# Optimization experiments

Hardware: AMD Instinct MI355X
Metric: run time of the kernel (lower is better)

Reference implementation:

```python
import jax, jax.numpy as jnp
import numpy as np
import math

N = 12288
IN_MAIN, IN_MOD = 64, 128
NC_INNER, NC_QK, OUT_MAIN = 16, 8, 64

def setup_inputs() -> dict:
    key = jax.random.key(0)
    ks = jax.random.split(key, 8)
    s = lambda fan_in: 1.0 / np.sqrt(fan_in)
    return {
        "x_main": jax.random.normal(ks[0], (N, IN_MAIN), dtype=jnp.float32),
        "x_mod": jax.random.normal(ks[1], (N, IN_MOD), dtype=jnp.float32),
        "xyz": jax.random.uniform(ks[2], (N, 3), dtype=jnp.float32),
        # MLP E: [in_main+in_mod -> nc_inner -> nc_inner], bias=False (weights stored [in, out])
        "W_e1": jax.random.uniform(ks[3], (IN_MAIN + IN_MOD, NC_INNER), jnp.float32, -s(IN_MAIN + IN_MOD), s(IN_MAIN + IN_MOD)),
        "W_e2": jax.random.uniform(ks[4], (NC_INNER, NC_INNER), jnp.float32, -s(NC_INNER), s(NC_INNER)),
        "W_q": jax.random.uniform(ks[5], (NC_INNER, NC_QK), jnp.float32, -s(NC_INNER), s(NC_INNER)),
        "W_k": jax.random.uniform(ks[6], (NC_INNER, NC_QK), jnp.float32, -s(NC_INNER), s(NC_INNER)),
        "W_v": jax.random.uniform(ks[7], (NC_INNER, OUT_MAIN), jnp.float32, -s(NC_INNER), s(NC_INNER)),
    }

def reference(x_main, x_mod, xyz, W_e1, W_e2, W_q, W_k, W_v):
    # concat 3D + 2D features: [N, in_main+in_mod]
    x = jnp.concatenate((x_main, x_mod), axis=-1)
    # MLP E (bias-free Linear + ReLU per layer): [N, nc_inner]
    h = jax.nn.relu(jax.nn.relu(x @ W_e1) @ W_e2)
    Q = h @ W_q  # [N, nc_qk]
    K = h @ W_k  # [N, nc_qk]
    V = h @ W_v  # [N, out_main]
    scale = 1.0 / math.sqrt(NC_QK)
    scores = (Q @ K.T) * scale          # [N, N] full global attention
    attn = jax.nn.softmax(scores, axis=1)
    return attn @ V                     # [N, out_main]
```

## Files before the change

### kernel.cpp

```cpp
#include <hip/hip_runtime.h>
#include <stdint.h>


#define NN 12288

typedef float    f32x16 __attribute__((ext_vector_type(16)));
typedef short    s16x8  __attribute__((ext_vector_type(8)));
typedef unsigned short u16;

#define MFMA_32x32x16_BF16 __builtin_amdgcn_mfma_f32_32x32x16_bf16

#define OFF_QB   0u
#define OFF_KB   196608u
#define OFF_VT   393216u
#define OFF_PO   2162688u

typedef __attribute__((address_space(3))) void lds_void_t;
typedef const __attribute__((address_space(1))) void gbl_void_t;
__device__ __forceinline__ void gld16(const void* g, void* l) {
    __builtin_amdgcn_global_load_lds((gbl_void_t*)g, (lds_void_t*)l, 16, 0, 0);
}

__device__ __forceinline__ float bf2f(u16 s) {
    union { unsigned int u; float f; } c; c.u = ((unsigned int)s) << 16; return c.f;
}
__device__ __forceinline__ u16 f2bf(float f) {
    union { float f; unsigned int u; } c; c.f = f;
    return (u16)((c.u + 0x8000u) >> 16);
}
__device__ __forceinline__ unsigned int pk2(float a, float b) {
    union { float f; unsigned int u; } ca, cb; ca.f = a; cb.f = b;
    return ((ca.u + 0x8000u) >> 16) | ((cb.u + 0x8000u) & 0xffff0000u);
}
__device__ __forceinline__ unsigned int pkbf(float a, float b) {
#if __has_builtin(__builtin_amdgcn_cvt_pk_bf16_f32)
    auto r = __builtin_amdgcn_cvt_pk_bf16_f32(a, b);
    union { decltype(r) v; unsigned int u; } c; c.v = r; return c.u;
#else
    return pk2(a, b);
#endif
}
__device__ __forceinline__ f32x16 zf16() {
    f32x16 z;
#pragma unroll
    for (int i = 0; i < 16; ++i) z[i] = 0.f;
    return z;
}
__device__ __forceinline__ s16x8 zs8() {
    s16x8 z;
#pragma unroll
    for (int i = 0; i < 8; ++i) z[i] = 0;
    return z;
}

union U8 { s16x8 v; unsigned int u[4]; };

__global__ __launch_bounds__(256) void k1_qkv(
    const void* __restrict__ xmain, const void* __restrict__ xmod,
    const void* __restrict__ we1, const void* __restrict__ we2,
    const void* __restrict__ wqp, const void* __restrict__ wkp,
    const void* __restrict__ wvp,
    u16* __restrict__ qb, u16* __restrict__ kb, u16* __restrict__ vt)
{
    __shared__ float wf[4608];
    __shared__ int   sflag;
    __shared__ float lh1[64][4][17];
    __shared__ float lh2[64][17];

    const int t = threadIdx.x;
    const int r = t >> 2;
    const int p = t & 3;
    const int row = blockIdx.x * 64 + r;

    if (t == 0) sflag = 0;
    __syncthreads();
    {
        float v = bf2f(((const u16*)xmod)[2 * t]);
        if (fabsf(v) > 16.f) atomicAdd(&sflag, 1);
    }
    __syncthreads();
    const int isf32 = (sflag > 8);

    const float SCL = 0.51006979f;
    if (isf32) {
        const float* a1 = (const float*)we1; const float* a2 = (const float*)we2;
        const float* aq = (const float*)wqp; const float* ak = (const float*)wkp;
        const float* av = (const float*)wvp;
        for (int i = t; i < 4608; i += 256) {
            if      (i < 3072) wf[i] = a1[i];
            else if (i < 3328) wf[i] = a2[i - 3072];
            else if (i < 3456) wf[i] = aq[i - 3328] * SCL;
            else if (i < 3584) wf[i] = ak[i - 3456];
            else               wf[i] = av[i - 3584];
        }
    } else {
        const u16* a1 = (const u16*)we1; const u16* a2 = (const u16*)we2;
        const u16* aq = (const u16*)wqp; const u16* ak = (const u16*)wkp;
        const u16* av = (const u16*)wvp;
        for (int i = t; i < 4608; i += 256) {
            if      (i < 3072) wf[i] = bf2f(a1[i]);
            else if (i < 3328) wf[i] = bf2f(a2[i - 3072]);
            else if (i < 3456) wf[i] = bf2f(aq[i - 3328]) * SCL;
            else if (i < 3584) wf[i] = bf2f(ak[i - 3456]);
            else               wf[i] = bf2f(av[i - 3584]);
        }
    }
    __syncthreads();

    const float* __restrict__ W1 = wf;
    const float* __restrict__ W2 = wf + 3072;
    const float* __restrict__ Wq = wf + 3328;
    const float* __restrict__ Wk = wf + 3456;
    const float* __restrict__ Wv = wf + 3584;

    float h1p[16];
#pragma unroll
    for (int o = 0; o < 16; ++o) h1p[o] = 0.f;

    if (isf32) {
#pragma unroll
        for (int cc = 0; cc < 12; ++cc) {
            const int c = p + cc * 4;
            float4 xv = (c < 16)
                ? ((const float4*)xmain)[(size_t)row * 16 + c]
                : ((const float4*)xmod)[(size_t)row * 32 + (c - 16)];
            float xs[4] = {xv.x, xv.y, xv.z, xv.w};
#pragma unroll
            for (int j = 0; j < 4; ++j) {
                const float* wr = W1 + (c * 4 + j) * 16;
#pragma unroll
                for (int o = 0; o < 16; ++o) h1p[o] += xs[j] * wr[o];
            }
        }
    } else {
#pragma unroll
        for (int cc = 0; cc < 12; ++cc) {
            const int c = p + cc * 4;
            uint2 xv = (c < 16)
                ? ((const uint2*)xmain)[(size_t)row * 16 + c]
                : ((const uint2*)xmod)[(size_t)row * 32 + (c - 16)];
            float xs[4] = { bf2f((u16)(xv.x & 0xffff)), bf2f((u16)(xv.x >> 16)),
                            bf2f((u16)(xv.y & 0xffff)), bf2f((u16)(xv.y >> 16)) };
#pragma unroll
            for (int j = 0; j < 4; ++j) {
                const float* wr = W1 + (c * 4 + j) * 16;
#pragma unroll
                for (int o = 0; o < 16; ++o) h1p[o] += xs[j] * wr[o];
            }
        }
    }
#pragma unroll
    for (int o = 0; o < 16; ++o) lh1[r][p][o] = h1p[o];
    __syncthreads();

    float h1[16];
#pragma unroll
    for (int o = 0; o < 16; ++o)
        h1[o] = fmaxf(lh1[r][0][o] + lh1[r][1][o] + lh1[r][2][o] + lh1[r][3][o], 0.f);

#pragma unroll
    for (int oo = 0; oo < 4; ++oo) {
        const int o = p * 4 + oo;
        float s = 0.f;
#pragma unroll
        for (int j = 0; j < 16; ++j) s += h1[j] * W2[j * 16 + o];
        lh2[r][o] = fmaxf(s, 0.f);
    }
    __syncthreads();

    float h2[16];
#pragma unroll
    for (int j = 0; j < 16; ++j) h2[j] = lh2[r][j];

    {
        float q0 = 0.f, q1 = 0.f, k0 = 0.f, k1 = 0.f;
        const int o = 2 * p;
#pragma unroll
        for (int j = 0; j < 16; ++j) {
            q0 += h2[j] * Wq[j * 8 + o];
            q1 += h2[j] * Wq[j * 8 + o + 1];
            k0 += h2[j] * Wk[j * 8 + o];
            k1 += h2[j] * Wk[j * 8 + o + 1];
        }
        ((unsigned int*)qb)[(size_t)row * 4 + p] = pk2(q0, q1);
        ((unsigned int*)kb)[(size_t)row * 4 + p] = pk2(k0, k1);
    }

    const int tI = row >> 5, kk = row & 31;
#pragma unroll
    for (int c16 = 0; c16 < 16; ++c16) {
        const int c = p * 16 + c16;
        float v = 0.f;
#pragma unroll
        for (int j = 0; j < 16; ++j) v += h2[j] * Wv[j * 64 + c];
        vt[(size_t)tI * 2304 + c * 36 + kk] = f2bf(v);
    }
}

__global__ __launch_bounds__(256, 6) void k2_attn(
    const u16* __restrict__ qb, const u16* __restrict__ kb,
    const u16* __restrict__ vt,
    u16* __restrict__ po, float* __restrict__ pl,
    int nsplit, int tiles)
{
    __shared__ union SM {
        uint4 stage[2][288];
        float sf[2304];
    } sm;

    const int tid  = threadIdx.x;
    const int lane = tid & 63;
    const int half = lane >> 5;
    const int l31  = lane & 31;
    const int w    = tid >> 6;
    const int qB   = (blockIdx.x % 96) * 128;
    const int sp   = blockIdx.x / 96;
    const int myq  = qB + 32 * w;
    const int key_start = sp * (NN / nsplit);
    const int t0 = key_start >> 5;

    const f32x16 Z = zf16();
    s16x8 qf = zs8();
    if (!half) qf = *(const s16x8*)(qb + (size_t)(myq + l31) * 8);

    f32x16 acc0 = Z, acc1 = Z;
    float ls = 0.f;

    {
        const char* g = (const char*)vt + (size_t)t0 * 4608 + 1152 * w + lane * 16;
        char* l = (char*)&sm.stage[0][0] + 1152 * w;
        gld16(g, l);
        if (lane < 8) gld16(g + 1024, l + 1024);
    }
    s16x8 ka_c = *(const s16x8*)(kb + (size_t)(key_start + l31) * 8);

    for (int kt = 0; kt < tiles; ++kt) {
        __builtin_amdgcn_s_waitcnt(0x0F70);
        __syncthreads();
        const int cb = kt & 1;
        const bool has_next = (kt + 1 < tiles);

        s16x8 ka_n;
        if (has_next) {
            ka_n = *(const s16x8*)(kb + (size_t)(key_start + (kt + 1) * 32 + l31) * 8);
            const char* g = (const char*)vt + (size_t)(t0 + kt + 1) * 4608
                          + 1152 * w + lane * 16;
            char* l = (char*)&sm.stage[cb ^ 1][0] + 1152 * w;
            gld16(g, l);
            if (lane < 8) gld16(g + 1024, l + 1024);
        }

        f32x16 S = MFMA_32x32x16_BF16(ka_c, qf, Z, 0, 0, 0);

        float pr[16];
        float ls0 = 0.f, ls1 = 0.f;
#pragma unroll
        for (int r = 0; r < 8; ++r) {
            pr[r]     = __builtin_amdgcn_exp2f(S[r]);
            pr[r + 8] = __builtin_amdgcn_exp2f(S[r + 8]);
            ls0 += pr[r];
            ls1 += pr[r + 8];
        }
        ls += ls0 + ls1;

        U8 pb0, pb1;
#pragma unroll
        for (int i = 0; i < 4; ++i) {
            pb0.u[i] = pkbf(pr[2 * i],     pr[2 * i + 1]);
            pb1.u[i] = pkbf(pr[8 + 2 * i], pr[8 + 2 * i + 1]);
        }

        const u16* base = (const u16*)&sm.stage[cb][0];
        const u16* r0 = base + l31 * 36 + 4 * half;
        const u16* r1 = base + (32 + l31) * 36 + 4 * half;
        U8 va;
        uint2 x0, x1;
        x0 = *(const uint2*)(r0);       x1 = *(const uint2*)(r0 + 8);
        va.u[0] = x0.x; va.u[1] = x0.y; va.u[2] = x1.x; va.u[3] = x1.y;
        acc0 = MFMA_32x32x16_BF16(va.v, pb0.v, acc0, 0, 0, 0);
        x0 = *(const uint2*)(r1);       x1 = *(const uint2*)(r1 + 8);
        va.u[0] = x0.x; va.u[1] = x0.y; va.u[2] = x1.x; va.u[3] = x1.y;
        acc1 = MFMA_32x32x16_BF16(va.v, pb0.v, acc1, 0, 0, 0);
        x0 = *(const uint2*)(r0 + 16);  x1 = *(const uint2*)(r0 + 24);
        va.u[0] = x0.x; va.u[1] = x0.y; va.u[2] = x1.x; va.u[3] = x1.y;
        acc0 = MFMA_32x32x16_BF16(va.v, pb1.v, acc0, 0, 0, 0);
        x0 = *(const uint2*)(r1 + 16);  x1 = *(const uint2*)(r1 + 24);
        va.u[0] = x0.x; va.u[1] = x0.y; va.u[2] = x1.x; va.u[3] = x1.y;
        acc1 = MFMA_32x32x16_BF16(va.v, pb1.v, acc1, 0, 0, 0);

        if (has_next) ka_c = ka_n;
    }

    ls += __shfl_xor(ls, 32, 64);

    u16* poS = po + (size_t)sp * (NN * 64);
    for (int j = 0; j < 4; ++j) {
        __syncthreads();
        if (w == j) {
#pragma unroll
            for (int r = 0; r < 16; ++r) {
                const int c = (r & 3) + 8 * (r >> 2) + 4 * half;
                sm.sf[c * 33 + l31]        = acc0[r];
                sm.sf[(32 + c) * 33 + l31] = acc1[r];
            }
            if (lane < 32) sm.sf[2112 + l31] = ls;
        }
        __syncthreads();
        const int rq = tid >> 3;
        const int c0 = (tid & 7) * 8;
        unsigned int u0 = pkbf(sm.sf[(c0 + 0) * 33 + rq], sm.sf[(c0 + 1) * 33 + rq]);
        unsigned int u1 = pkbf(sm.sf[(c0 + 2) * 33 + rq], sm.sf[(c0 + 3) * 33 + rq]);
        unsigned int u2 = pkbf(sm.sf[(c0 + 4) * 33 + rq], sm.sf[(c0 + 5) * 33 + rq]);
        unsigned int u3 = pkbf(sm.sf[(c0 + 6) * 33 + rq], sm.sf[(c0 + 7) * 33 + rq]);
        *(uint4*)(poS + (size_t)(qB + 32 * j + rq) * 64 + c0) =
            make_uint4(u0, u1, u2, u3);
        if (tid < 32)
            pl[(size_t)sp * NN + qB + 32 * j + tid] = sm.sf[2112 + tid];
    }
}

__global__ __launch_bounds__(256) void k3_norm(
    const u16* __restrict__ po, const float* __restrict__ pl,
    float4* __restrict__ out, int nsplit)
{
    const int i = blockIdx.x * 256 + threadIdx.x;
    const int row = i >> 4;
    const int c0 = (i & 15) * 4;
    float l = 0.f;
    float o0 = 0.f, o1 = 0.f, o2 = 0.f, o3 = 0.f;
    for (int s = 0; s < nsplit; ++s) {
        l += pl[(size_t)s * NN + row];
        uint2 p = *(const uint2*)(po + (size_t)s * (NN * 64) +
                                  (size_t)row * 64 + c0);
        o0 += bf2f((u16)(p.x & 0xffff)); o1 += bf2f((u16)(p.x >> 16));
        o2 += bf2f((u16)(p.y & 0xffff)); o3 += bf2f((u16)(p.y >> 16));
    }
    const float rl = 1.0f / l;
    out[i] = make_float4(o0 * rl, o1 * rl, o2 * rl, o3 * rl);
}

extern "C" void kernel_launch(void* const* d_in, const int* in_sizes, int n_in,
                              void* d_out, int out_size, void* d_ws, size_t ws_size,
                              hipStream_t stream)
{
    const void* xmain = d_in[0];
    const void* xmod  = d_in[1];
    const void* we1   = d_in[3];
    const void* we2   = d_in[4];
    const void* wq    = d_in[5];
    const void* wk    = d_in[6];
    const void* wv    = d_in[7];

    char* ws = (char*)d_ws;
    u16*   qb   = (u16*)  (ws + OFF_QB);
    u16*   kb   = (u16*)  (ws + OFF_KB);
    u16*   vt   = (u16*)  (ws + OFF_VT);

    int S = 1;
    for (int cand = 16; cand >= 1; cand >>= 1) {
        size_t need = (size_t)OFF_PO + (size_t)cand * (NN * 64 * 2) +
                      (size_t)cand * (NN * 4);
        if (ws_size >= need) { S = cand; break; }
    }
    u16*   po = (u16*)(ws + OFF_PO);
    float* pl = (float*)(ws + OFF_PO + (size_t)S * (NN * 64 * 2));
    const int tiles = NN / (32 * S);

    k1_qkv<<<192, 256, 0, stream>>>(xmain, xmod, we1, we2, wq, wk, wv,
                                    qb, kb, vt);
    k2_attn<<<96 * S, 256, 0, stream>>>(qb, kb, vt, po, pl, S, tiles);
    k3_norm<<<768, 256, 0, stream>>>(po, pl, (float4*)d_out, S);
}
```

Measured before the change: 131.2 us.

## Process two query tiles per wave to reuse staged V and K fragments

Each attention wave now handles 64 queries (two 32-row Q fragments), so every K fragment load and every staged V tile in LDS feeds twice as many MFMAs. The grid halves to 48*S blocks and the occupancy hint drops from 6 to 2 to leave room for four accumulators. The QKV projection kernel is also re-split to 32 rows per block with 8 threads per row, giving more blocks. The trade is fewer resident waves and a longer per-wave dependency chain, in exchange for less LDS and global traffic per unit of work.

```diff
diff --git a/kernel.cpp b/kernel.cpp
--- a/kernel.cpp
+++ b/kernel.cpp
@@ -64,13 +64,13 @@
 {
     __shared__ float wf[4608];
     __shared__ int   sflag;
-    __shared__ float lh1[64][4][17];
-    __shared__ float lh2[64][17];
+    __shared__ float lh1[32][8][17];
+    __shared__ float lh2[32][17];
 
     const int t = threadIdx.x;
-    const int r = t >> 2;
-    const int p = t & 3;
-    const int row = blockIdx.x * 64 + r;
+    const int r = t >> 3;
+    const int p = t & 7;
+    const int row = blockIdx.x * 32 + r;
 
     if (t == 0) sflag = 0;
     __syncthreads();
@@ -119,8 +119,8 @@
 
     if (isf32) {
 #pragma unroll
-        for (int cc = 0; cc < 12; ++cc) {
-            const int c = p + cc * 4;
+        for (int cc = 0; cc < 6; ++cc) {
+            const int c = p + cc * 8;
             float4 xv = (c < 16)
                 ? ((const float4*)xmain)[(size_t)row * 16 + c]
                 : ((const float4*)xmod)[(size_t)row * 32 + (c - 16)];
@@ -134,8 +134,8 @@
         }
     } else {
 #pragma unroll
-        for (int cc = 0; cc < 12; ++cc) {
-            const int c = p + cc * 4;
+        for (int cc = 0; cc < 6; ++cc) {
+            const int c = p + cc * 8;
             uint2 xv = (c < 16)
                 ? ((const uint2*)xmain)[(size_t)row * 16 + c]
                 : ((const uint2*)xmod)[(size_t)row * 32 + (c - 16)];
@@ -155,12 +155,16 @@
 
     float h1[16];
 #pragma unroll
-    for (int o = 0; o < 16; ++o)
-        h1[o] = fmaxf(lh1[r][0][o] + lh1[r][1][o] + lh1[r][2][o] + lh1[r][3][o], 0.f);
-
-#pragma unroll
-    for (int oo = 0; oo < 4; ++oo) {
-        const int o = p * 4 + oo;
+    for (int o = 0; o < 16; ++o) {
+        float s = lh1[r][0][o];
+#pragma unroll
+        for (int q = 1; q < 8; ++q) s += lh1[r][q][o];
+        h1[o] = fmaxf(s, 0.f);
+    }
+
+#pragma unroll
+    for (int oo = 0; oo < 2; ++oo) {
+        const int o = p * 2 + oo;
         float s = 0.f;
 #pragma unroll
         for (int j = 0; j < 16; ++j) s += h1[j] * W2[j * 16 + o];
@@ -173,23 +177,23 @@
     for (int j = 0; j < 16; ++j) h2[j] = lh2[r][j];
 
     {
-        float q0 = 0.f, q1 = 0.f, k0 = 0.f, k1 = 0.f;
-        const int o = 2 * p;
+        const int isK = p >> 2;
+        const int o = 2 * (p & 3);
+        const float* Wx = isK ? Wk : Wq;
+        float a0 = 0.f, a1 = 0.f;
 #pragma unroll
         for (int j = 0; j < 16; ++j) {
-            q0 += h2[j] * Wq[j * 8 + o];
-            q1 += h2[j] * Wq[j * 8 + o + 1];
-            k0 += h2[j] * Wk[j * 8 + o];
-            k1 += h2[j] * Wk[j * 8 + o + 1];
-        }
-        ((unsigned int*)qb)[(size_t)row * 4 + p] = pk2(q0, q1);
-        ((unsigned int*)kb)[(size_t)row * 4 + p] = pk2(k0, k1);
+            a0 += h2[j] * Wx[j * 8 + o];
+            a1 += h2[j] * Wx[j * 8 + o + 1];
+        }
+        unsigned int* dst = isK ? (unsigned int*)kb : (unsigned int*)qb;
+        dst[(size_t)row * 4 + (p & 3)] = pk2(a0, a1);
     }
 
     const int tI = row >> 5, kk = row & 31;
 #pragma unroll
-    for (int c16 = 0; c16 < 16; ++c16) {
-        const int c = p * 16 + c16;
+    for (int c8 = 0; c8 < 8; ++c8) {
+        const int c = p * 8 + c8;
         float v = 0.f;
 #pragma unroll
         for (int j = 0; j < 16; ++j) v += h2[j] * Wv[j * 64 + c];
@@ -197,7 +201,7 @@
     }
 }
 
-__global__ __launch_bounds__(256, 6) void k2_attn(
+__global__ __launch_bounds__(256, 2) void k2_attn(
     const u16* __restrict__ qb, const u16* __restrict__ kb,
     const u16* __restrict__ vt,
     u16* __restrict__ po, float* __restrict__ pl,
@@ -213,18 +217,21 @@
     const int half = lane >> 5;
     const int l31  = lane & 31;
     const int w    = tid >> 6;
-    const int qB   = (blockIdx.x % 96) * 128;
-    const int sp   = blockIdx.x / 96;
-    const int myq  = qB + 32 * w;
+    const int qB   = (blockIdx.x % 48) * 256;
+    const int sp   = blockIdx.x / 48;
+    const int myq  = qB + 64 * w;
     const int key_start = sp * (NN / nsplit);
     const int t0 = key_start >> 5;
 
     const f32x16 Z = zf16();
-    s16x8 qf = zs8();
-    if (!half) qf = *(const s16x8*)(qb + (size_t)(myq + l31) * 8);
-
-    f32x16 acc0 = Z, acc1 = Z;
-    float ls = 0.f;
+    s16x8 qf0 = zs8(), qf1 = zs8();
+    if (!half) {
+        qf0 = *(const s16x8*)(qb + (size_t)(myq + l31) * 8);
+        qf1 = *(const s16x8*)(qb + (size_t)(myq + 32 + l31) * 8);
+    }
+
+    f32x16 acc00 = Z, acc01 = Z, acc10 = Z, acc11 = Z;
+    float ls0 = 0.f, ls1 = 0.f;
 
     {
         const char* g = (const char*)vt + (size_t)t0 * 4608 + 1152 * w + lane * 16;
@@ -250,60 +257,85 @@
             if (lane < 8) gld16(g + 1024, l + 1024);
         }
 
-        f32x16 S = MFMA_32x32x16_BF16(ka_c, qf, Z, 0, 0, 0);
-
-        float pr[16];
-        float ls0 = 0.f, ls1 = 0.f;
-#pragma unroll
-        for (int r = 0; r < 8; ++r) {
-            pr[r]     = __builtin_amdgcn_exp2f(S[r]);
-            pr[r + 8] = __builtin_amdgcn_exp2f(S[r + 8]);
-            ls0 += pr[r];
-            ls1 += pr[r + 8];
-        }
-        ls += ls0 + ls1;
-
-        U8 pb0, pb1;
-#pragma unroll
-        for (int i = 0; i < 4; ++i) {
-            pb0.u[i] = pkbf(pr[2 * i],     pr[2 * i + 1]);
-            pb1.u[i] = pkbf(pr[8 + 2 * i], pr[8 + 2 * i + 1]);
-        }
-
         const u16* base = (const u16*)&sm.stage[cb][0];
         const u16* r0 = base + l31 * 36 + 4 * half;
         const u16* r1 = base + (32 + l31) * 36 + 4 * half;
-        U8 va;
-        uint2 x0, x1;
-        x0 = *(const uint2*)(r0);       x1 = *(const uint2*)(r0 + 8);
-        va.u[0] = x0.x; va.u[1] = x0.y; va.u[2] = x1.x; va.u[3] = x1.y;
-        acc0 = MFMA_32x32x16_BF16(va.v, pb0.v, acc0, 0, 0, 0);
-        x0 = *(const uint2*)(r1);       x1 = *(const uint2*)(r1 + 8);
-        va.u[0] = x0.x; va.u[1] = x0.y; va.u[2] = x1.x; va.u[3] = x1.y;
-        acc1 = MFMA_32x32x16_BF16(va.v, pb0.v, acc1, 0, 0, 0);
-        x0 = *(const uint2*)(r0 + 16);  x1 = *(const uint2*)(r0 + 24);
-        va.u[0] = x0.x; va.u[1] = x0.y; va.u[2] = x1.x; va.u[3] = x1.y;
-        acc0 = MFMA_32x32x16_BF16(va.v, pb1.v, acc0, 0, 0, 0);
-        x0 = *(const uint2*)(r1 + 16);  x1 = *(const uint2*)(r1 + 24);
-        va.u[0] = x0.x; va.u[1] = x0.y; va.u[2] = x1.x; va.u[3] = x1.y;
-        acc1 = MFMA_32x32x16_BF16(va.v, pb1.v, acc1, 0, 0, 0);
+        U8 vaA0, vaA1, vaB0, vaB1;
+        {
+            uint2 x0, x1;
+            x0 = *(const uint2*)(r0);       x1 = *(const uint2*)(r0 + 8);
+            vaA0.u[0] = x0.x; vaA0.u[1] = x0.y; vaA0.u[2] = x1.x; vaA0.u[3] = x1.y;
+            x0 = *(const uint2*)(r1);       x1 = *(const uint2*)(r1 + 8);
+            vaA1.u[0] = x0.x; vaA1.u[1] = x0.y; vaA1.u[2] = x1.x; vaA1.u[3] = x1.y;
+            x0 = *(const uint2*)(r0 + 16);  x1 = *(const uint2*)(r0 + 24);
+            vaB0.u[0] = x0.x; vaB0.u[1] = x0.y; vaB0.u[2] = x1.x; vaB0.u[3] = x1.y;
+            x0 = *(const uint2*)(r1 + 16);  x1 = *(const uint2*)(r1 + 24);
+            vaB1.u[0] = x0.x; vaB1.u[1] = x0.y; vaB1.u[2] = x1.x; vaB1.u[3] = x1.y;
+        }
+
+        {
+            f32x16 S = MFMA_32x32x16_BF16(ka_c, qf0, Z, 0, 0, 0);
+            float pr[16];
+            float a = 0.f, b = 0.f;
+#pragma unroll
+            for (int r = 0; r < 8; ++r) {
+                pr[r]     = __builtin_amdgcn_exp2f(S[r]);
+                pr[r + 8] = __builtin_amdgcn_exp2f(S[r + 8]);
+                a += pr[r]; b += pr[r + 8];
+            }
+            ls0 += a + b;
+            U8 pbA, pbB;
+#pragma unroll
+            for (int i = 0; i < 4; ++i) {
+                pbA.u[i] = pkbf(pr[2 * i],     pr[2 * i + 1]);
+                pbB.u[i] = pkbf(pr[8 + 2 * i], pr[8 + 2 * i + 1]);
+            }
+            acc00 = MFMA_32x32x16_BF16(vaA0.v, pbA.v, acc00, 0, 0, 0);
+            acc01 = MFMA_32x32x16_BF16(vaA1.v, pbA.v, acc01, 0, 0, 0);
+            acc00 = MFMA_32x32x16_BF16(vaB0.v, pbB.v, acc00, 0, 0, 0);
+            acc01 = MFMA_32x32x16_BF16(vaB1.v, pbB.v, acc01, 0, 0, 0);
+        }
+        {
+            f32x16 S = MFMA_32x32x16_BF16(ka_c, qf1, Z, 0, 0, 0);
+            float pr[16];
+            float a = 0.f, b = 0.f;
+#pragma unroll
+            for (int r = 0; r < 8; ++r) {
+                pr[r]     = __builtin_amdgcn_exp2f(S[r]);
+                pr[r + 8] = __builtin_amdgcn_exp2f(S[r + 8]);
+                a += pr[r]; b += pr[r + 8];
+            }
+            ls1 += a + b;
+            U8 pbA, pbB;
+#pragma unroll
+            for (int i = 0; i < 4; ++i) {
+                pbA.u[i] = pkbf(pr[2 * i],     pr[2 * i + 1]);
+                pbB.u[i] = pkbf(pr[8 + 2 * i], pr[8 + 2 * i + 1]);
+            }
+            acc10 = MFMA_32x32x16_BF16(vaA0.v, pbA.v, acc10, 0, 0, 0);
+            acc11 = MFMA_32x32x16_BF16(vaA1.v, pbA.v, acc11, 0, 0, 0);
+            acc10 = MFMA_32x32x16_BF16(vaB0.v, pbB.v, acc10, 0, 0, 0);
+            acc11 = MFMA_32x32x16_BF16(vaB1.v, pbB.v, acc11, 0, 0, 0);
+        }
 
         if (has_next) ka_c = ka_n;
     }
 
-    ls += __shfl_xor(ls, 32, 64);
+    ls0 += __shfl_xor(ls0, 32, 64);
+    ls1 += __shfl_xor(ls1, 32, 64);
 
     u16* poS = po + (size_t)sp * (NN * 64);
-    for (int j = 0; j < 4; ++j) {
+    for (int j = 0; j < 8; ++j) {
         __syncthreads();
-        if (w == j) {
+        if (w == (j >> 1)) {
+            const int f = j & 1;
 #pragma unroll
             for (int r = 0; r < 16; ++r) {
                 const int c = (r & 3) + 8 * (r >> 2) + 4 * half;
-                sm.sf[c * 33 + l31]        = acc0[r];
-                sm.sf[(32 + c) * 33 + l31] = acc1[r];
-            }
-            if (lane < 32) sm.sf[2112 + l31] = ls;
+                sm.sf[c * 33 + l31]        = f ? acc10[r] : acc00[r];
+                sm.sf[(32 + c) * 33 + l31] = f ? acc11[r] : acc01[r];
+            }
+            if (lane < 32) sm.sf[2112 + l31] = f ? ls1 : ls0;
         }
         __syncthreads();
         const int rq = tid >> 3;
@@ -366,8 +398,8 @@
     float* pl = (float*)(ws + OFF_PO + (size_t)S * (NN * 64 * 2));
     const int tiles = NN / (32 * S);
 
-    k1_qkv<<<192, 256, 0, stream>>>(xmain, xmod, we1, we2, wq, wk, wv,
+    k1_qkv<<<384, 256, 0, stream>>>(xmain, xmod, we1, we2, wq, wk, wv,
                                     qb, kb, vt);
-    k2_attn<<<96 * S, 256, 0, stream>>>(qb, kb, vt, po, pl, S, tiles);
+    k2_attn<<<48 * S, 256, 0, stream>>>(qb, kb, vt, po, pl, S, tiles);
     k3_norm<<<768, 256, 0, stream>>>(po, pl, (float4*)d_out, S);
 }
```

Result: slower. 139.5 us (+6.3%).
